# Performance work log

Measured on AMD Instinct MI355X. Metric: run time of the kernel, lower is better.

## Reference

```python
import jax, jax.numpy as jnp
import numpy as np

INPUT, HIDDEN, OUTPUT, SEQ = 128, 128, 128, 2048
BATCH = 256

def setup_inputs() -> dict:
    key = jax.random.key(0)
    ks = jax.random.split(key, 6)
    s_x = 1.0 / np.sqrt(INPUT)
    s_h = 1.0 / np.sqrt(HIDDEN)
    return {
        "x": jax.random.normal(ks[0], (BATCH, SEQ, INPUT), jnp.float32),
        "h0": jnp.zeros((BATCH, HIDDEN), jnp.float32),
        # weights stored as [in, out] so forward is x @ W + b (same math as torch Linear)
        "W_xh": jax.random.uniform(ks[1], (INPUT, HIDDEN), jnp.float32, -s_x, s_x),
        "b_xh": jax.random.uniform(ks[2], (HIDDEN,), jnp.float32, -s_x, s_x),
        "W_hh": jax.random.uniform(ks[3], (HIDDEN, HIDDEN), jnp.float32, -s_h, s_h),
        "W_out": jax.random.uniform(ks[4], (HIDDEN, OUTPUT), jnp.float32, -s_h, s_h),
        "b_out": jax.random.uniform(ks[5], (OUTPUT,), jnp.float32, -s_h, s_h),
    }

def reference(x, h0, W_xh, b_xh, W_hh, W_out, b_out):
    # Precompute input projections for all timesteps in one big GEMM: [B,S,H]
    xh = jnp.einsum("bsi,ih->bsh", x, W_xh) + b_xh

    def step(h, xh_t):
        h = jnp.tanh(xh_t + h @ W_hh)
        return h, None

    # scan over time (strict sequential dependency)
    h_last, _ = jax.lax.scan(step, h0, jnp.swapaxes(xh, 0, 1))  # [S,B,H] scan
    # module returns only the last timestep's output projection
    return h_last @ W_out + b_out
```

## Files before the change

### kernel.cpp

```cpp
#include <hip/hip_runtime.h>
#include <hip/hip_bf16.h>


#define SEQ   2048
#define HID   128
#define BATCH 256
#define BD    16

typedef __attribute__((ext_vector_type(8))) short    short8;
typedef __attribute__((ext_vector_type(4))) float    f32x4;
typedef __attribute__((ext_vector_type(4))) float    f4;
typedef __attribute__((ext_vector_type(2))) unsigned u32x2;
typedef __attribute__((ext_vector_type(4))) unsigned u32x4;

union F8 { unsigned u[4]; short8 s; };

__device__ __forceinline__ unsigned pkbf(float a, float b) {
    union { __hip_bfloat16 h[2]; unsigned u; } t;
    t.h[0] = __float2bfloat16(a);
    t.h[1] = __float2bfloat16(b);
    return t.u;
}

__device__ __forceinline__ float blo(unsigned u) {
    union { unsigned v; float f; } t; t.v = u << 16; return t.f;
}
__device__ __forceinline__ float bhi(unsigned u) {
    union { unsigned v; float f; } t; t.v = u & 0xffff0000u; return t.f;
}

__device__ __forceinline__ float tanh_fast(float x) {
    float e = __builtin_amdgcn_exp2f(x * 2.8853900817779268f);
    return 1.0f - 2.0f * __builtin_amdgcn_rcpf(e + 1.0f);
}

__device__ __forceinline__ void block_sync() {
    asm volatile("s_waitcnt lgkmcnt(0)" ::: "memory");
    __builtin_amdgcn_s_barrier();
    asm volatile("" ::: "memory");
}

#define MFMA16(A,B,C) __builtin_amdgcn_mfma_f32_16x16x32_bf16((A),(B),(C),0,0,0)

__launch_bounds__(256, 1)
__global__ void xh_gemm_kernel(const float* __restrict__ x,
                               const float* __restrict__ Wxh,
                               const float* __restrict__ bxh,
                               __hip_bfloat16* __restrict__ xh)
{
    const int tid  = threadIdx.x;
    const int wv   = tid >> 6;
    const int lane = tid & 63;
    const int lg   = lane >> 4;
    const int lm   = lane & 15;

    const int gw = blockIdx.x * 4 + wv;
    const int NW = gridDim.x * 4;
    const int NT = (BATCH * SEQ) / 16;

    short8 wa[8][4];
    {
        #pragma unroll
        for (int T = 0; T < 8; ++T) {
            #pragma unroll
            for (int c = 0; c < 4; ++c) {
                F8 f;
                #pragma unroll
                for (int e2 = 0; e2 < 4; ++e2) {
                    int k = 32*c + 8*lg + 2*e2;
                    f.u[e2] = pkbf(Wxh[(size_t)k*HID + 16*T + lm],
                                   Wxh[(size_t)(k+1)*HID + 16*T + lm]);
                }
                wa[T][c] = f.s;
            }
        }
    }
    float bb[8][4];
    #pragma unroll
    for (int T = 0; T < 8; ++T)
        #pragma unroll
        for (int r = 0; r < 4; ++r)
            bb[T][r] = bxh[16*T + 4*lg + r];

    for (int tile = gw; tile < NT; tile += NW) {
        const float* xp = x + (size_t)tile*16*HID + (size_t)lm*HID + 8*lg;
        f4 s[8];
        #pragma unroll
        for (int c = 0; c < 4; ++c) {
            s[2*c]   = *(const f4*)(xp + 32*c);
            s[2*c+1] = *(const f4*)(xp + 32*c + 4);
        }
        F8 xf[4];
        #pragma unroll
        for (int c = 0; c < 4; ++c) {
            xf[c].u[0] = pkbf(s[2*c][0],   s[2*c][1]);
            xf[c].u[1] = pkbf(s[2*c][2],   s[2*c][3]);
            xf[c].u[2] = pkbf(s[2*c+1][0], s[2*c+1][1]);
            xf[c].u[3] = pkbf(s[2*c+1][2], s[2*c+1][3]);
        }
        __hip_bfloat16* op = xh + (size_t)(tile*16 + lm) * HID;
        #pragma unroll
        for (int T = 0; T < 8; ++T) {
            f32x4 acc = {bb[T][0], bb[T][1], bb[T][2], bb[T][3]};
            #pragma unroll
            for (int c = 0; c < 4; ++c)
                acc = MFMA16(wa[T][c], xf[c].s, acc);
            u32x2 w;
            w[0] = pkbf(acc[0], acc[1]);
            w[1] = pkbf(acc[2], acc[3]);
            *reinterpret_cast<u32x2*>(op + 16*T + 4*lg) = w;
        }
    }
}


#define REC8W_STEP(S, P, POFF, TRT)                                           \
    {                                                                          \
        f32x4 a;                                                               \
        a[0] = blo(S[0]); a[1] = bhi(S[0]);                                    \
        a[2] = blo(S[1]); a[3] = bhi(S[1]);                                    \
        if ((TRT) + 4 < SEQ) S = *(const u32x2*)(xq + (POFF)*256);             \
        block_sync();                       \
        const char* rb = lds + (P)*4096;                                       \
        short8 f0 = *(const short8*)(rb + 0*1024 + lane*16);                   \
        short8 f1 = *(const short8*)(rb + 1*1024 + lane*16);                   \
        short8 f2 = *(const short8*)(rb + 2*1024 + lane*16);                   \
        short8 f3 = *(const short8*)(rb + 3*1024 + lane*16);                   \
        f32x4 tacc = {0.f, 0.f, 0.f, 0.f};                                     \
        a    = MFMA16(whf[0], f0, a);                                          \
        tacc = MFMA16(whf[2], f2, tacc);                                       \
        a    = MFMA16(whf[1], f1, a);                                          \
        tacc = MFMA16(whf[3], f3, tacc);                                       \
        a += tacc;                                                             \
        u32x2 nf;                                                              \
        nf[0] = pkbf(tanh_fast(a[0]), tanh_fast(a[1]));                        \
        nf[1] = pkbf(tanh_fast(a[2]), tanh_fast(a[3]));                        \
        *reinterpret_cast<u32x2*>(lds + ((P)^1)*4096 + wr) = nf;               \
    }

__launch_bounds__(512, 1)
__global__ void rnn_rec8w_kernel(const __hip_bfloat16* __restrict__ xh,
                                 const float* __restrict__ h0,
                                 const float* __restrict__ Whh,
                                 const float* __restrict__ Wout,
                                 const float* __restrict__ bout,
                                 float* __restrict__ out)
{
    __shared__ __align__(16) char lds[2 * 4096];

    const int tid  = threadIdx.x;
    const int wv   = tid >> 6;
    const int jw   = wv & 3;
    const int u    = wv >> 2;
    const int lane = tid & 63;
    const int lg   = lane >> 4;
    const int lm   = lane & 15;
    const int b0   = blockIdx.x * BD;

    short8 whf[4];
    {
        const int scol = 32*jw + 8*(lm >> 2) + 4*u + (lm & 3);
        #pragma unroll
        for (int c = 0; c < 4; ++c) {
            F8 f;
            #pragma unroll
            for (int e2 = 0; e2 < 4; ++e2) {
                int k = 32*c + 8*lg + 2*e2;
                f.u[e2] = pkbf(Whh[(size_t)k*HID + scol],
                               Whh[(size_t)(k+1)*HID + scol]);
            }
            whf[c] = f.s;
        }
    }

    const int wr = jw*1024 + lane*16 + 8*u;

    {
        const float* hp = h0 + (size_t)(b0 + lm) * HID + 32*jw + 8*lg + 4*u;
        f4 v = *(const f4*)(hp);
        u32x2 iv;
        iv[0] = pkbf(v[0], v[1]);
        iv[1] = pkbf(v[2], v[3]);
        *reinterpret_cast<u32x2*>(lds + wr) = iv;
    }

    const char* xq = (const char*)xh + (size_t)(b0 + lm) * SEQ * 256
                   + (size_t)(32*jw + 8*lg + 4*u) * 2;

    u32x2 sA = *(const u32x2*)(xq + 0*256);
    u32x2 sB = *(const u32x2*)(xq + 1*256);
    u32x2 sC = *(const u32x2*)(xq + 2*256);
    u32x2 sD = *(const u32x2*)(xq + 3*256);

    for (int t = 0; t < SEQ; t += 4) {
        REC8W_STEP(sA, 0, 4, t);
        REC8W_STEP(sB, 1, 5, t + 1);
        REC8W_STEP(sC, 0, 6, t + 2);
        REC8W_STEP(sD, 1, 7, t + 3);
        xq += 4 * 256;
    }

    block_sync();
    {
        const int T = wv;
        short8 h0f = *reinterpret_cast<const short8*>(lds + 0*1024 + lane*16);
        short8 h1f = *reinterpret_cast<const short8*>(lds + 1*1024 + lane*16);
        short8 h2f = *reinterpret_cast<const short8*>(lds + 2*1024 + lane*16);
        short8 h3f = *reinterpret_cast<const short8*>(lds + 3*1024 + lane*16);

        f32x4 o = {bout[16*T + 4*lg + 0], bout[16*T + 4*lg + 1],
                   bout[16*T + 4*lg + 2], bout[16*T + 4*lg + 3]};
        #pragma unroll
        for (int c = 0; c < 4; ++c) {
            F8 f;
            #pragma unroll
            for (int e2 = 0; e2 < 4; ++e2) {
                int k = 32*c + 8*lg + 2*e2;
                f.u[e2] = pkbf(Wout[(size_t)k*HID + 16*T + lm],
                               Wout[(size_t)(k+1)*HID + 16*T + lm]);
            }
            const short8 hf = (c == 0) ? h0f : (c == 1) ? h1f : (c == 2) ? h2f : h3f;
            o = MFMA16(f.s, hf, o);
        }
        float* op = out + (size_t)(b0 + lm) * HID + 16*T + 4*lg;
        *reinterpret_cast<f4*>(op) = o;
    }
}

#define RNN_STEP(SLOT, P, POFF, TRT)                                          \
    {                                                                          \
        F8 xf[4];                                                              \
        _Pragma("unroll")                                                      \
        for (int c = 0; c < 4; ++c) {                                          \
            xf[c].u[0] = pkbf(SLOT[2*c][0],   SLOT[2*c][1]);                   \
            xf[c].u[1] = pkbf(SLOT[2*c][2],   SLOT[2*c][3]);                   \
            xf[c].u[2] = pkbf(SLOT[2*c+1][0], SLOT[2*c+1][1]);                 \
            xf[c].u[3] = pkbf(SLOT[2*c+1][2], SLOT[2*c+1][3]);                 \
        }                                                                      \
        if ((TRT) + 2 < SEQ) {                                                 \
            _Pragma("unroll")                                                  \
            for (int c = 0; c < 4; ++c) {                                      \
                SLOT[2*c]   = *(const f4*)(xq + (POFF)*HID + 32*c);            \
                SLOT[2*c+1] = *(const f4*)(xq + (POFF)*HID + 32*c + 4);        \
            }                                                                  \
        }                                                                      \
        f32x4 a0 = {bx[0][0], bx[0][1], bx[0][2], bx[0][3]};                   \
        f32x4 a1 = {bx[1][0], bx[1][1], bx[1][2], bx[1][3]};                   \
        _Pragma("unroll")                                                      \
        for (int c = 0; c < 4; ++c) {                                          \
            a0 = MFMA16(wxh[0][c], xf[c].s, a0);                               \
            a1 = MFMA16(wxh[1][c], xf[c].s, a1);                               \
        }                                                                      \
        block_sync();                                                          \
        _Pragma("unroll")                                                      \
        for (int c = 0; c < 4; ++c) {                                          \
            short8 hf = *reinterpret_cast<const short8*>(lds + (P)*4096 + rd[c]); \
            a0 = MFMA16(whh[0][c], hf, a0);                                    \
            a1 = MFMA16(whh[1][c], hf, a1);                                    \
        }                                                                      \
        u32x2 w0, w1;                                                          \
        w0[0] = pkbf(tanh_fast(a0[0]), tanh_fast(a0[1]));                      \
        w0[1] = pkbf(tanh_fast(a0[2]), tanh_fast(a0[3]));                      \
        w1[0] = pkbf(tanh_fast(a1[0]), tanh_fast(a1[1]));                      \
        w1[1] = pkbf(tanh_fast(a1[2]), tanh_fast(a1[3]));                      \
        *reinterpret_cast<u32x2*>(lds + ((P)^1)*4096 + hw[0]) = w0;            \
        *reinterpret_cast<u32x2*>(lds + ((P)^1)*4096 + hw[1]) = w1;            \
    }

__launch_bounds__(256, 1)
__global__ void rnn_fused_kernel(const float* __restrict__ x,
                                 const float* __restrict__ h0,
                                 const float* __restrict__ Wxh,
                                 const float* __restrict__ bxh,
                                 const float* __restrict__ Whh,
                                 const float* __restrict__ Wout,
                                 const float* __restrict__ bout,
                                 float* __restrict__ out)
{
    __shared__ __align__(16) char lds[2 * 4096];

    const int tid  = threadIdx.x;
    const int wv   = tid >> 6;
    const int lane = tid & 63;
    const int lg   = lane >> 4;
    const int lm   = lane & 15;
    const int b0   = blockIdx.x * BD;

    short8 wxh[2][4], whh[2][4];
    {
        const int col = 32*wv + lm;
        #pragma unroll
        for (int T = 0; T < 2; ++T) {
            #pragma unroll
            for (int c = 0; c < 4; ++c) {
                F8 fx, fh;
                #pragma unroll
                for (int e2 = 0; e2 < 4; ++e2) {
                    int k = 32*c + 8*lg + 2*e2;
                    fx.u[e2] = pkbf(Wxh[(size_t)k*HID + col + 16*T],
                                    Wxh[(size_t)(k+1)*HID + col + 16*T]);
                    fh.u[e2] = pkbf(Whh[(size_t)k*HID + col + 16*T],
                                    Whh[(size_t)(k+1)*HID + col + 16*T]);
                }
                wxh[T][c] = fx.s; whh[T][c] = fh.s;
            }
        }
    }
    float bx[2][4];
    #pragma unroll
    for (int T = 0; T < 2; ++T)
        #pragma unroll
        for (int r = 0; r < 4; ++r)
            bx[T][r] = bxh[32*wv + 16*T + 4*lg + r];

    int rd[4];
    #pragma unroll
    for (int c = 0; c < 4; ++c)
        rd[c] = (lm*256 + 64*c + 16*lg) ^ ((lm & 7) << 4);
    int hw[2];
    #pragma unroll
    for (int T = 0; T < 2; ++T)
        hw[T] = (lm*256 + 2*(32*wv + 16*T + 4*lg)) ^ ((lm & 7) << 4);

    {
        int b  = tid >> 4;
        int j0 = (tid & 15) * 8;
        const float* hp = h0 + (size_t)(b0 + b) * HID + j0;
        f4 v0 = *(const f4*)(hp);
        f4 v1 = *(const f4*)(hp + 4);
        F8 f;
        f.u[0] = pkbf(v0[0], v0[1]); f.u[1] = pkbf(v0[2], v0[3]);
        f.u[2] = pkbf(v1[0], v1[1]); f.u[3] = pkbf(v1[2], v1[3]);
        int off = (b*256 + 2*j0) ^ ((b & 7) << 4);
        *reinterpret_cast<short8*>(lds + off) = f.s;
    }

    const float* xq = x + (size_t)(b0 + lm) * SEQ * HID + 8*lg;
    f4 sA[8], sB[8];
    #pragma unroll
    for (int c = 0; c < 4; ++c) {
        sA[2*c]   = *(const f4*)(xq + 32*c);
        sA[2*c+1] = *(const f4*)(xq + 32*c + 4);
        sB[2*c]   = *(const f4*)(xq + HID + 32*c);
        sB[2*c+1] = *(const f4*)(xq + HID + 32*c + 4);
    }

    for (int t = 0; t < SEQ; t += 2) {
        RNN_STEP(sA, 0, 2, t);
        RNN_STEP(sB, 1, 3, t + 1);
        xq += 2 * HID;
    }

    block_sync();
    {
        short8 wo[2][4];
        const int col = 32*wv + lm;
        #pragma unroll
        for (int T = 0; T < 2; ++T) {
            #pragma unroll
            for (int c = 0; c < 4; ++c) {
                F8 f;
                #pragma unroll
                for (int e2 = 0; e2 < 4; ++e2) {
                    int k = 32*c + 8*lg + 2*e2;
                    f.u[e2] = pkbf(Wout[(size_t)k*HID + col + 16*T],
                                   Wout[(size_t)(k+1)*HID + col + 16*T]);
                }
                wo[T][c] = f.s;
            }
        }
        f32x4 o0 = {bout[32*wv + 4*lg + 0], bout[32*wv + 4*lg + 1],
                    bout[32*wv + 4*lg + 2], bout[32*wv + 4*lg + 3]};
        f32x4 o1 = {bout[32*wv + 16 + 4*lg + 0], bout[32*wv + 16 + 4*lg + 1],
                    bout[32*wv + 16 + 4*lg + 2], bout[32*wv + 16 + 4*lg + 3]};
        #pragma unroll
        for (int c = 0; c < 4; ++c) {
            short8 hf = *reinterpret_cast<const short8*>(lds + rd[c]);
            o0 = MFMA16(wo[0][c], hf, o0);
            o1 = MFMA16(wo[1][c], hf, o1);
        }
        float* op = out + (size_t)(b0 + lm) * HID + 32*wv + 4*lg;
        *reinterpret_cast<f4*>(op)      = o0;
        *reinterpret_cast<f4*>(op + 16) = o1;
    }
}

extern "C" void kernel_launch(void* const* d_in, const int* in_sizes, int n_in,
                              void* d_out, int out_size, void* d_ws, size_t ws_size,
                              hipStream_t stream) {
    const float* x    = (const float*)d_in[0];
    const float* h0   = (const float*)d_in[1];
    const float* Wxh  = (const float*)d_in[2];
    const float* bxh  = (const float*)d_in[3];
    const float* Whh  = (const float*)d_in[4];
    const float* Wout = (const float*)d_in[5];
    const float* bout = (const float*)d_in[6];
    (void)in_sizes; (void)n_in; (void)out_size;

    const size_t need = (size_t)BATCH * SEQ * HID * 2;
    if (ws_size >= need) {
        __hip_bfloat16* xh = (__hip_bfloat16*)d_ws;
        xh_gemm_kernel<<<dim3(512), dim3(256), 0, stream>>>(x, Wxh, bxh, xh);
        rnn_rec8w_kernel<<<dim3(BATCH / BD), dim3(512), 0, stream>>>(
            xh, h0, Whh, Wout, bout, (float*)d_out);
    } else {
        rnn_fused_kernel<<<dim3(BATCH / BD), dim3(256), 0, stream>>>(
            x, h0, Wxh, bxh, Whh, Wout, bout, (float*)d_out);
    }
}
```

Before: 904.5 us.

## Pack two batch tiles per 1024-thread block and split MFMA accumulation chains

The recurrence kernel now processes two 16-row batch tiles per block with 16 waves (8 per tile), each tile using its own LDS double buffer, so half as many blocks are launched. The four MFMAs per step now accumulate into four independent accumulators instead of two chains, which shortens the dependency chain on the serial critical path. The risk is that each block-wide barrier now spans 16 waves across both tiles, so a slow wave in one tile stalls the other, and fewer blocks means fewer CUs are in use.

```diff
diff --git a/kernel.cpp b/kernel.cpp
--- a/kernel.cpp
+++ b/kernel.cpp
@@ -114,48 +114,53 @@
 }
 
 
-#define REC8W_STEP(S, P, POFF, TRT)                                           \
+#define REC16W_STEP(S, P, POFF, TRT)                                          \
     {                                                                          \
         f32x4 a;                                                               \
         a[0] = blo(S[0]); a[1] = bhi(S[0]);                                    \
         a[2] = blo(S[1]); a[3] = bhi(S[1]);                                    \
         if ((TRT) + 4 < SEQ) S = *(const u32x2*)(xq + (POFF)*256);             \
-        block_sync();                       \
-        const char* rb = lds + (P)*4096;                                       \
+        block_sync();         \
+        const char* rb = zbase + (P)*4096;                                     \
         short8 f0 = *(const short8*)(rb + 0*1024 + lane*16);                   \
         short8 f1 = *(const short8*)(rb + 1*1024 + lane*16);                   \
         short8 f2 = *(const short8*)(rb + 2*1024 + lane*16);                   \
         short8 f3 = *(const short8*)(rb + 3*1024 + lane*16);                   \
-        f32x4 tacc = {0.f, 0.f, 0.f, 0.f};                                     \
-        a    = MFMA16(whf[0], f0, a);                                          \
-        tacc = MFMA16(whf[2], f2, tacc);                                       \
-        a    = MFMA16(whf[1], f1, a);                                          \
-        tacc = MFMA16(whf[3], f3, tacc);                                       \
-        a += tacc;                                                             \
+        f32x4 t1 = {0.f,0.f,0.f,0.f};                                          \
+        f32x4 t2 = {0.f,0.f,0.f,0.f};                                          \
+        f32x4 t3 = {0.f,0.f,0.f,0.f};                                          \
+        a  = MFMA16(whf[0], f0, a);                                            \
+        t1 = MFMA16(whf[1], f1, t1);                                           \
+        t2 = MFMA16(whf[2], f2, t2);                                           \
+        t3 = MFMA16(whf[3], f3, t3);                                           \
+        a += (t1 + t2) + t3;                                                   \
         u32x2 nf;                                                              \
         nf[0] = pkbf(tanh_fast(a[0]), tanh_fast(a[1]));                        \
         nf[1] = pkbf(tanh_fast(a[2]), tanh_fast(a[3]));                        \
-        *reinterpret_cast<u32x2*>(lds + ((P)^1)*4096 + wr) = nf;               \
-    }
-
-__launch_bounds__(512, 1)
-__global__ void rnn_rec8w_kernel(const __hip_bfloat16* __restrict__ xh,
-                                 const float* __restrict__ h0,
-                                 const float* __restrict__ Whh,
-                                 const float* __restrict__ Wout,
-                                 const float* __restrict__ bout,
-                                 float* __restrict__ out)
+        *reinterpret_cast<u32x2*>(zbase + ((P)^1)*4096 + wr) = nf;             \
+    }
+
+__launch_bounds__(1024, 1)
+__global__ void rnn_rec16w_kernel(const __hip_bfloat16* __restrict__ xh,
+                                  const float* __restrict__ h0,
+                                  const float* __restrict__ Whh,
+                                  const float* __restrict__ Wout,
+                                  const float* __restrict__ bout,
+                                  float* __restrict__ out)
 {
-    __shared__ __align__(16) char lds[2 * 4096];
+    __shared__ __align__(16) char lds[2 * 8192];
 
     const int tid  = threadIdx.x;
     const int wv   = tid >> 6;
+    const int ti   = wv >> 3;
     const int jw   = wv & 3;
-    const int u    = wv >> 2;
+    const int u    = (wv >> 2) & 1;
     const int lane = tid & 63;
     const int lg   = lane >> 4;
     const int lm   = lane & 15;
-    const int b0   = blockIdx.x * BD;
+    const int b0   = blockIdx.x * 32;
+
+    char* zbase = lds + ti * 8192;
 
     short8 whf[4];
     {
@@ -176,15 +181,15 @@
     const int wr = jw*1024 + lane*16 + 8*u;
 
     {
-        const float* hp = h0 + (size_t)(b0 + lm) * HID + 32*jw + 8*lg + 4*u;
+        const float* hp = h0 + (size_t)(b0 + 16*ti + lm) * HID + 32*jw + 8*lg + 4*u;
         f4 v = *(const f4*)(hp);
         u32x2 iv;
         iv[0] = pkbf(v[0], v[1]);
         iv[1] = pkbf(v[2], v[3]);
-        *reinterpret_cast<u32x2*>(lds + wr) = iv;
-    }
-
-    const char* xq = (const char*)xh + (size_t)(b0 + lm) * SEQ * 256
+        *reinterpret_cast<u32x2*>(zbase + wr) = iv;
+    }
+
+    const char* xq = (const char*)xh + (size_t)(b0 + 16*ti + lm) * SEQ * 256
                    + (size_t)(32*jw + 8*lg + 4*u) * 2;
 
     u32x2 sA = *(const u32x2*)(xq + 0*256);
@@ -193,20 +198,20 @@
     u32x2 sD = *(const u32x2*)(xq + 3*256);
 
     for (int t = 0; t < SEQ; t += 4) {
-        REC8W_STEP(sA, 0, 4, t);
-        REC8W_STEP(sB, 1, 5, t + 1);
-        REC8W_STEP(sC, 0, 6, t + 2);
-        REC8W_STEP(sD, 1, 7, t + 3);
+        REC16W_STEP(sA, 0, 4, t);
+        REC16W_STEP(sB, 1, 5, t + 1);
+        REC16W_STEP(sC, 0, 6, t + 2);
+        REC16W_STEP(sD, 1, 7, t + 3);
         xq += 4 * 256;
     }
 
     block_sync();
     {
-        const int T = wv;
-        short8 h0f = *reinterpret_cast<const short8*>(lds + 0*1024 + lane*16);
-        short8 h1f = *reinterpret_cast<const short8*>(lds + 1*1024 + lane*16);
-        short8 h2f = *reinterpret_cast<const short8*>(lds + 2*1024 + lane*16);
-        short8 h3f = *reinterpret_cast<const short8*>(lds + 3*1024 + lane*16);
+        const int T = wv & 7;
+        short8 h0f = *reinterpret_cast<const short8*>(zbase + 0*1024 + lane*16);
+        short8 h1f = *reinterpret_cast<const short8*>(zbase + 1*1024 + lane*16);
+        short8 h2f = *reinterpret_cast<const short8*>(zbase + 2*1024 + lane*16);
+        short8 h3f = *reinterpret_cast<const short8*>(zbase + 3*1024 + lane*16);
 
         f32x4 o = {bout[16*T + 4*lg + 0], bout[16*T + 4*lg + 1],
                    bout[16*T + 4*lg + 2], bout[16*T + 4*lg + 3]};
@@ -222,7 +227,7 @@
             const short8 hf = (c == 0) ? h0f : (c == 1) ? h1f : (c == 2) ? h2f : h3f;
             o = MFMA16(f.s, hf, o);
         }
-        float* op = out + (size_t)(b0 + lm) * HID + 16*T + 4*lg;
+        float* op = out + (size_t)(b0 + 16*ti + lm) * HID + 16*T + 4*lg;
         *reinterpret_cast<f4*>(op) = o;
     }
 }
@@ -401,7 +406,7 @@
     if (ws_size >= need) {
         __hip_bfloat16* xh = (__hip_bfloat16*)d_ws;
         xh_gemm_kernel<<<dim3(512), dim3(256), 0, stream>>>(x, Wxh, bxh, xh);
-        rnn_rec8w_kernel<<<dim3(BATCH / BD), dim3(512), 0, stream>>>(
+        rnn_rec16w_kernel<<<dim3(BATCH / 32), dim3(1024), 0, stream>>>(
             xh, h0, Whh, Wout, bout, (float*)d_out);
     } else {
         rnn_fused_kernel<<<dim3(BATCH / BD), dim3(256), 0, stream>>>(
```

Measured after the change: 1.210 ms. 1.34x slower.
